# Optimization experiments

Hardware: AMD Instinct MI355X
Metric: run time of the kernel (lower is better)

The kernel has to match this reference:

```python
import jax, jax.numpy as jnp
import numpy as np

S_STATES, C_TYPES, G_GENES = 16, 64, 20000


def setup_inputs() -> dict:
    key = jax.random.key(0)
    k1, k2, k3, k4 = jax.random.split(key, 4)
    Z_mu = jax.random.normal(k1, (C_TYPES, G_GENES), dtype=jnp.float32)
    # positive log-normal sigmas, moderate scale for numerical stability
    Z_sigma = jax.random.uniform(k2, (C_TYPES, G_GENES), dtype=jnp.float32) * 0.5 + 0.1
    # build a valid correlation matrix (PSD with unit diagonal) so var >= 0
    L = jax.random.normal(k3, (C_TYPES, C_TYPES), dtype=jnp.float32)
    cov = L @ L.T + C_TYPES * jnp.eye(C_TYPES, dtype=jnp.float32)
    d = jnp.sqrt(jnp.diag(cov))
    corr = cov / (d[:, None] * d[None, :])
    # cell_prob rows on the simplex (Dirichlet-like), per state
    cell_prob = jax.nn.softmax(jax.random.normal(k4, (S_STATES, C_TYPES), dtype=jnp.float32), axis=1)
    return {"Z_mu": Z_mu, "Z_sigma": Z_sigma, "corr": corr, "cell_prob": cell_prob}


def reference(Z_mu, Z_sigma, corr, cell_prob):
    """Vectorized LogNorm.calculate_mu_sigma.

    Z_mu, Z_sigma: (C, G); corr: (C, C); cell_prob: (S, C).
    Returns mu, sigma of shape (S, G) -- moment-matched log-normal sum params
    for every (state, gene) pair, matching the nested-loop torch original.
    """
    # EV[s,c,g] = exp(mu + sigma^2/2) * w  (first moment of each component, weighted)
    ev_base = jnp.exp(Z_mu + 0.5 * Z_sigma ** 2)            # (C, G)
    EV = cell_prob[:, :, None] * ev_base[None, :, :]         # (S, C, G)
    Ssum = EV.sum(axis=1)                                    # (S, G)
    # A[s,c,g] = EV * sigma; var = sum_{c,d} A_c corr_{cd} A_d / Ssum^2
    A = EV * Z_sigma[None, :, :]                             # (S, C, G)
    var = jnp.einsum('scg,cd,sdg->sg', A, corr, A) / (Ssum ** 2)  # (S, G)
    mu_s = jnp.log(Ssum) - 0.5 * var
    sigma_s = jnp.sqrt(var)
    return (mu_s, sigma_s)
```

## Files before the change

### kernel.cpp

```cpp
#include <hip/hip_runtime.h>


#define S_STATES 16
#define C_TYPES  64
#define G_GENES  20000
#define OUT_HALF (S_STATES * G_GENES)
#define NPAIR    96
#define PER_WAVE 12

typedef _Float16 f16x2 __attribute__((ext_vector_type(2)));
typedef _Float16 f16x8 __attribute__((ext_vector_type(8)));
typedef float    f32x4 __attribute__((ext_vector_type(4)));

union Frag8 { f16x2 p[4]; f16x8 v; uint4 u; _Float16 h[8]; };

__global__ __launch_bounds__(64)
void build_A(const float* __restrict__ corr, const float* __restrict__ w,
             unsigned short* __restrict__ cwA)
{
    const int p    = blockIdx.x;
    const int lane = threadIdx.x;
    const int gl   = lane & 15;
    const int q    = lane >> 4;
    Frag8 v;
    if (p < NPAIR) {
        const int dh = (p >= 64);
        const int c  = dh ? p - 32 : p;
        const int d0 = dh * 32 + q * 8;
        const float wc = w[gl * C_TYPES + c];
        const float4 c0 = *(const float4*)(corr + c * C_TYPES + d0);
        const float4 c1 = *(const float4*)(corr + c * C_TYPES + d0 + 4);
        const float4 w0 = *(const float4*)(w + gl * C_TYPES + d0);
        const float4 w1 = *(const float4*)(w + gl * C_TYPES + d0 + 4);
        const float cv[8] = {c0.x,c0.y,c0.z,c0.w,c1.x,c1.y,c1.z,c1.w};
        const float wv[8] = {w0.x,w0.y,w0.z,w0.w,w1.x,w1.y,w1.z,w1.w};
#pragma unroll
        for (int j = 0; j < 8; ++j) {
            const int d = d0 + j;
            const float sc = (d < c) ? 2.0f : (d == c ? 1.0f : 0.0f);
            v.h[j] = (_Float16)(sc * cv[j] * wc * wv[j]);
        }
    } else {
        const int k0 = (p - NPAIR) * 32 + q * 8;
        const float4 w0 = *(const float4*)(w + gl * C_TYPES + k0);
        const float4 w1 = *(const float4*)(w + gl * C_TYPES + k0 + 4);
        const float wv[8] = {w0.x,w0.y,w0.z,w0.w,w1.x,w1.y,w1.z,w1.w};
#pragma unroll
        for (int j = 0; j < 8; ++j) v.h[j] = (_Float16)wv[j];
    }
    *(uint4*)(cwA + (p << 9) + lane * 8) = v.u;
}

__global__ __launch_bounds__(512, 4)
void lognorm_main(const float* __restrict__ Z_mu,
                  const float* __restrict__ Z_sigma,
                  const unsigned short* __restrict__ cwA,
                  float* __restrict__ out)
{
    __shared__ f16x2 x2pT[32][35];
    __shared__ f16x2 x1pT[32][35];
    __shared__ f16x2 x2tp[C_TYPES][21];
    __shared__ float accs[8][S_STATES][33];
    __shared__ float ssum_s[S_STATES][33];

    const int gt    = blockIdx.x;
    const int tid   = threadIdx.x;
    const int w     = tid >> 6;
    const int lane  = tid & 63;
    const int gl    = lane & 15;
    const int q     = lane >> 4;
    const int gbase = gt * 32;

    Frag8 afr[PER_WAVE];
    {
        const unsigned short* Abase = cwA + (w << 9) + lane * 8;
#pragma unroll
        for (int i = 0; i < PER_WAVE; ++i)
            afr[i].u = *(const uint4*)(Abase + (i << 12));
    }
    Frag8 wf0, wf1;
    if (w < 2) {
        wf0.u = *(const uint4*)(cwA + ((NPAIR + 0) << 9) + lane * 8);
        wf1.u = *(const uint4*)(cwA + ((NPAIR + 1) << 9) + lane * 8);
    }

    {
        const int dp = tid >> 4;
        const int gq = tid & 15;
        const float* zm = Z_mu    + (2*dp) * G_GENES + gbase + gq;
        const float* zs = Z_sigma + (2*dp) * G_GENES + gbase + gq;
        const float m00 = zm[0], m01 = zm[16];
        const float m10 = zm[G_GENES], m11 = zm[G_GENES + 16];
        const float s00 = zs[0], s01 = zs[16];
        const float s10 = zs[G_GENES], s11 = zs[G_GENES + 16];
        const float e00 = __expf(fmaf(0.5f*s00, s00, m00)) * 0.25f;
        const float e01 = __expf(fmaf(0.5f*s01, s01, m01)) * 0.25f;
        const float e10 = __expf(fmaf(0.5f*s10, s10, m10)) * 0.25f;
        const float e11 = __expf(fmaf(0.5f*s11, s11, m11)) * 0.25f;
        const float x200 = e00*s00, x201 = e01*s01;
        const float x210 = e10*s10, x211 = e11*s11;
        f16x2 a;
        a.x = (_Float16)x200; a.y = (_Float16)x210; x2pT[gq][dp]      = a;
        a.x = (_Float16)x201; a.y = (_Float16)x211; x2pT[gq + 16][dp] = a;
        a.x = (_Float16)e00;  a.y = (_Float16)e10;  x1pT[gq][dp]      = a;
        a.x = (_Float16)e01;  a.y = (_Float16)e11;  x1pT[gq + 16][dp] = a;
        a.x = (_Float16)x200; a.y = (_Float16)x201; x2tp[2*dp][gq]    = a;
        a.x = (_Float16)x210; a.y = (_Float16)x211; x2tp[2*dp+1][gq]  = a;
    }
    __syncthreads();

    f16x2 xh[2][4][2];
#pragma unroll
    for (int dh = 0; dh < 2; ++dh)
#pragma unroll
        for (int t = 0; t < 2; ++t)
#pragma unroll
            for (int jp = 0; jp < 4; ++jp)
                xh[dh][jp][t] = x2pT[gl + 16*t][dh*16 + q*4 + jp];

    f16x2 xct[PER_WAVE];
#pragma unroll
    for (int i = 0; i < PER_WAVE; ++i) {
        const int c = i*8 + w - ((i >= 8) ? 32 : 0);
        xct[i] = x2tp[c][gl];
    }

    f32x4 acc0a = {0.f,0.f,0.f,0.f}, acc0b = {0.f,0.f,0.f,0.f};
    f32x4 acc1a = {0.f,0.f,0.f,0.f}, acc1b = {0.f,0.f,0.f,0.f};
#pragma unroll
    for (int i = 0; i < PER_WAVE; ++i) {
        const int dh = (i >= 8) ? 1 : 0;
        Frag8 b0, b1;
#pragma unroll
        for (int jp = 0; jp < 4; ++jp) {
            f16x2 s0; s0.x = xct[i].x; s0.y = xct[i].x;
            f16x2 s1; s1.x = xct[i].y; s1.y = xct[i].y;
            b0.p[jp] = s0 * xh[dh][jp][0];
            b1.p[jp] = s1 * xh[dh][jp][1];
        }
        if (i & 1) {
            acc0b = __builtin_amdgcn_mfma_f32_16x16x32_f16(afr[i].v, b0.v, acc0b, 0, 0, 0);
            acc1b = __builtin_amdgcn_mfma_f32_16x16x32_f16(afr[i].v, b1.v, acc1b, 0, 0, 0);
        } else {
            acc0a = __builtin_amdgcn_mfma_f32_16x16x32_f16(afr[i].v, b0.v, acc0a, 0, 0, 0);
            acc1a = __builtin_amdgcn_mfma_f32_16x16x32_f16(afr[i].v, b1.v, acc1a, 0, 0, 0);
        }
    }
    const f32x4 acc0 = acc0a + acc0b;
    const f32x4 acc1 = acc1a + acc1b;
#pragma unroll
    for (int r = 0; r < 4; ++r) {
        accs[w][q*4 + r][gl]      = acc0[r];
        accs[w][q*4 + r][gl + 16] = acc1[r];
    }

    if (w < 2) {
        Frag8 x1f[2];
#pragma unroll
        for (int kk = 0; kk < 2; ++kk)
#pragma unroll
            for (int jp = 0; jp < 4; ++jp)
                x1f[kk].p[jp] = x1pT[gl + 16*w][kk*16 + q*4 + jp];
        f32x4 sa = {0.f,0.f,0.f,0.f};
        sa = __builtin_amdgcn_mfma_f32_16x16x32_f16(wf0.v, x1f[0].v, sa, 0, 0, 0);
        sa = __builtin_amdgcn_mfma_f32_16x16x32_f16(wf1.v, x1f[1].v, sa, 0, 0, 0);
#pragma unroll
        for (int r = 0; r < 4; ++r) ssum_s[q*4 + r][gl + 16*w] = sa[r];
    }
    __syncthreads();

    const int s  = tid >> 5;
    const int gx = tid & 31;
    float vn = 0.f;
#pragma unroll
    for (int k = 0; k < 8; ++k) vn += accs[k][s][gx];
    const float ss   = ssum_s[s][gx];
    const float rvar = fmaxf(vn, 0.f) / (ss * ss);
    out[s * G_GENES + gbase + gx] =
        __logf(ss) + 1.3862943611f - 0.5f * rvar;
    out[OUT_HALF + s * G_GENES + gbase + gx] = sqrtf(rvar);
}

extern "C" void kernel_launch(void* const* d_in, const int* in_sizes, int n_in,
                              void* d_out, int out_size, void* d_ws, size_t ws_size,
                              hipStream_t stream) {
    const float* Z_mu      = (const float*)d_in[0];
    const float* Z_sigma   = (const float*)d_in[1];
    const float* corr      = (const float*)d_in[2];
    const float* cell_prob = (const float*)d_in[3];
    float* out = (float*)d_out;
    unsigned short* cwA = (unsigned short*)d_ws;

    build_A<<<dim3(NPAIR + 2), dim3(64), 0, stream>>>(corr, cell_prob, cwA);

    const int gtiles = G_GENES / 32;
    lognorm_main<<<dim3(gtiles), dim3(512), 0, stream>>>(
        Z_mu, Z_sigma, cwA, out);
}
```

Measured before the change: 16.58 us.

## Fuse A-fragment construction into main kernel, drop build_A launch

```diff
diff --git a/kernel.cpp b/kernel.cpp
--- a/kernel.cpp
+++ b/kernel.cpp
@@ -5,7 +5,6 @@
 #define C_TYPES  64
 #define G_GENES  20000
 #define OUT_HALF (S_STATES * G_GENES)
-#define NPAIR    96
 #define PER_WAVE 12
 
 typedef _Float16 f16x2 __attribute__((ext_vector_type(2)));
@@ -14,49 +13,14 @@
 
 union Frag8 { f16x2 p[4]; f16x8 v; uint4 u; _Float16 h[8]; };
 
-__global__ __launch_bounds__(64)
-void build_A(const float* __restrict__ corr, const float* __restrict__ w,
-             unsigned short* __restrict__ cwA)
+__global__ __launch_bounds__(512, 4)
+void lognorm_one(const float* __restrict__ Z_mu,
+                 const float* __restrict__ Z_sigma,
+                 const float* __restrict__ corr,
+                 const float* __restrict__ w,
+                 float* __restrict__ out)
 {
-    const int p    = blockIdx.x;
-    const int lane = threadIdx.x;
-    const int gl   = lane & 15;
-    const int q    = lane >> 4;
-    Frag8 v;
-    if (p < NPAIR) {
-        const int dh = (p >= 64);
-        const int c  = dh ? p - 32 : p;
-        const int d0 = dh * 32 + q * 8;
-        const float wc = w[gl * C_TYPES + c];
-        const float4 c0 = *(const float4*)(corr + c * C_TYPES + d0);
-        const float4 c1 = *(const float4*)(corr + c * C_TYPES + d0 + 4);
-        const float4 w0 = *(const float4*)(w + gl * C_TYPES + d0);
-        const float4 w1 = *(const float4*)(w + gl * C_TYPES + d0 + 4);
-        const float cv[8] = {c0.x,c0.y,c0.z,c0.w,c1.x,c1.y,c1.z,c1.w};
-        const float wv[8] = {w0.x,w0.y,w0.z,w0.w,w1.x,w1.y,w1.z,w1.w};
-#pragma unroll
-        for (int j = 0; j < 8; ++j) {
-            const int d = d0 + j;
-            const float sc = (d < c) ? 2.0f : (d == c ? 1.0f : 0.0f);
-            v.h[j] = (_Float16)(sc * cv[j] * wc * wv[j]);
-        }
-    } else {
-        const int k0 = (p - NPAIR) * 32 + q * 8;
-        const float4 w0 = *(const float4*)(w + gl * C_TYPES + k0);
-        const float4 w1 = *(const float4*)(w + gl * C_TYPES + k0 + 4);
-        const float wv[8] = {w0.x,w0.y,w0.z,w0.w,w1.x,w1.y,w1.z,w1.w};
-#pragma unroll
-        for (int j = 0; j < 8; ++j) v.h[j] = (_Float16)wv[j];
-    }
-    *(uint4*)(cwA + (p << 9) + lane * 8) = v.u;
-}
-
-__global__ __launch_bounds__(512, 4)
-void lognorm_main(const float* __restrict__ Z_mu,
-                  const float* __restrict__ Z_sigma,
-                  const unsigned short* __restrict__ cwA,
-                  float* __restrict__ out)
-{
+    __shared__ float mcf[C_TYPES][C_TYPES];
     __shared__ f16x2 x2pT[32][35];
     __shared__ f16x2 x1pT[32][35];
     __shared__ f16x2 x2tp[C_TYPES][21];
@@ -65,23 +29,25 @@
 
     const int gt    = blockIdx.x;
     const int tid   = threadIdx.x;
-    const int w     = tid >> 6;
+    const int w4    = tid >> 6;
     const int lane  = tid & 63;
     const int gl    = lane & 15;
     const int q     = lane >> 4;
     const int gbase = gt * 32;
 
-    Frag8 afr[PER_WAVE];
-    {
-        const unsigned short* Abase = cwA + (w << 9) + lane * 8;
+    float wdv[2][8];
 #pragma unroll
-        for (int i = 0; i < PER_WAVE; ++i)
-            afr[i].u = *(const uint4*)(Abase + (i << 12));
+    for (int dh = 0; dh < 2; ++dh) {
+        const float4 a = *(const float4*)(w + gl*C_TYPES + dh*32 + q*8);
+        const float4 b = *(const float4*)(w + gl*C_TYPES + dh*32 + q*8 + 4);
+        wdv[dh][0]=a.x; wdv[dh][1]=a.y; wdv[dh][2]=a.z; wdv[dh][3]=a.w;
+        wdv[dh][4]=b.x; wdv[dh][5]=b.y; wdv[dh][6]=b.z; wdv[dh][7]=b.w;
     }
-    Frag8 wf0, wf1;
-    if (w < 2) {
-        wf0.u = *(const uint4*)(cwA + ((NPAIR + 0) << 9) + lane * 8);
-        wf1.u = *(const uint4*)(cwA + ((NPAIR + 1) << 9) + lane * 8);
+    float wcv[PER_WAVE];
+#pragma unroll
+    for (int i = 0; i < PER_WAVE; ++i) {
+        const int c = i*8 + w4 - ((i >= 8) ? 32 : 0);
+        wcv[i] = w[gl*C_TYPES + c];
     }
 
     {
@@ -107,7 +73,32 @@
         a.x = (_Float16)x200; a.y = (_Float16)x201; x2tp[2*dp][gq]    = a;
         a.x = (_Float16)x210; a.y = (_Float16)x211; x2tp[2*dp+1][gq]  = a;
     }
+
+    {
+        const int c  = tid >> 3;
+        const int d0 = (tid & 7) * 8;
+        const float4 c0 = *(const float4*)(corr + c*C_TYPES + d0);
+        const float4 c1 = *(const float4*)(corr + c*C_TYPES + d0 + 4);
+        const float cv[8] = {c0.x,c0.y,c0.z,c0.w, c1.x,c1.y,c1.z,c1.w};
+#pragma unroll
+        for (int jj = 0; jj < 8; ++jj) {
+            const int d = d0 + jj;
+            const float sc = (d < c) ? 2.0f : (d == c ? 1.0f : 0.0f);
+            mcf[c][d] = sc * cv[jj];
+        }
+    }
     __syncthreads();
+
+    Frag8 afr[PER_WAVE];
+#pragma unroll
+    for (int i = 0; i < PER_WAVE; ++i) {
+        const int dh = (i >= 8) ? 1 : 0;
+        const int c  = i*8 + w4 - dh*32;
+        const float* mrow = &mcf[c][dh*32 + q*8];
+#pragma unroll
+        for (int j = 0; j < 8; ++j)
+            afr[i].h[j] = (_Float16)((mrow[j] * wcv[i]) * wdv[dh][j]);
+    }
 
     f16x2 xh[2][4][2];
 #pragma unroll
@@ -121,7 +112,7 @@
     f16x2 xct[PER_WAVE];
 #pragma unroll
     for (int i = 0; i < PER_WAVE; ++i) {
-        const int c = i*8 + w - ((i >= 8) ? 32 : 0);
+        const int c = i*8 + w4 - ((i >= 8) ? 32 : 0);
         xct[i] = x2tp[c][gl];
     }
 
@@ -150,22 +141,28 @@
     const f32x4 acc1 = acc1a + acc1b;
 #pragma unroll
     for (int r = 0; r < 4; ++r) {
-        accs[w][q*4 + r][gl]      = acc0[r];
-        accs[w][q*4 + r][gl + 16] = acc1[r];
+        accs[w4][q*4 + r][gl]      = acc0[r];
+        accs[w4][q*4 + r][gl + 16] = acc1[r];
     }
 
-    if (w < 2) {
+    if (w4 < 2) {
+        Frag8 wf0, wf1;
+#pragma unroll
+        for (int j = 0; j < 8; ++j) {
+            wf0.h[j] = (_Float16)w[gl*C_TYPES + q*8 + j];
+            wf1.h[j] = (_Float16)w[gl*C_TYPES + 32 + q*8 + j];
+        }
         Frag8 x1f[2];
 #pragma unroll
         for (int kk = 0; kk < 2; ++kk)
 #pragma unroll
             for (int jp = 0; jp < 4; ++jp)
-                x1f[kk].p[jp] = x1pT[gl + 16*w][kk*16 + q*4 + jp];
+                x1f[kk].p[jp] = x1pT[gl + 16*w4][kk*16 + q*4 + jp];
         f32x4 sa = {0.f,0.f,0.f,0.f};
         sa = __builtin_amdgcn_mfma_f32_16x16x32_f16(wf0.v, x1f[0].v, sa, 0, 0, 0);
         sa = __builtin_amdgcn_mfma_f32_16x16x32_f16(wf1.v, x1f[1].v, sa, 0, 0, 0);
 #pragma unroll
-        for (int r = 0; r < 4; ++r) ssum_s[q*4 + r][gl + 16*w] = sa[r];
+        for (int r = 0; r < 4; ++r) ssum_s[q*4 + r][gl + 16*w4] = sa[r];
     }
     __syncthreads();
 
@@ -189,11 +186,8 @@
     const float* corr      = (const float*)d_in[2];
     const float* cell_prob = (const float*)d_in[3];
     float* out = (float*)d_out;
-    unsigned short* cwA = (unsigned short*)d_ws;
-
-    build_A<<<dim3(NPAIR + 2), dim3(64), 0, stream>>>(corr, cell_prob, cwA);
 
     const int gtiles = G_GENES / 32;
-    lognorm_main<<<dim3(gtiles), dim3(512), 0, stream>>>(
-        Z_mu, Z_sigma, cwA, out);
+    lognorm_one<<<dim3(gtiles), dim3(512), 0, stream>>>(
+        Z_mu, Z_sigma, corr, cell_prob, out);
 }
```

New measurement: 17.83 us. 7.5% more time.
